# Performance work log

Measured on AMD Instinct MI355X. Metric: run time of the kernel, lower is better.

Reference implementation:

```python
import jax, jax.numpy as jnp
import numpy as np

B, S, HID, HEADS = 1, 2048, 4096, 32
HEAD_D = HID // HEADS
SCALE = float(1.0 / np.sqrt(HEAD_D))  # = 1/norm_factor^2 with use_mup=False


def setup_inputs() -> dict:
    key = jax.random.key(0)
    k0, k1, k2, k3, k4 = jax.random.split(key, 5)
    return {
        "x": jax.random.normal(k0, (B, S, HID), jnp.float32),
        "attn_qkvw": jax.random.normal(k1, (HID, 3 * HID), jnp.float32) * 0.02,
        "attn_qkvb": jax.random.normal(k2, (3 * HID,), jnp.float32) * 0.02,
        "attn_ow": jax.random.normal(k3, (HID, HID), jnp.float32) * 0.02,
        "attn_ob": jax.random.normal(k4, (HID,), jnp.float32) * 0.02,
    }


def reference(x, attn_qkvw, attn_qkvb, attn_ow, attn_ob):
    # QKV projection (LinearOp): [B,S,HID] @ [HID,3*HID] + bias -> packed qkv
    qkv = x @ attn_qkvw + attn_qkvb
    q, k, v = jnp.split(qkv, 3, axis=-1)  # each [B,S,HID]

    def to_heads(t):
        return t.reshape(B, S, HEADS, HEAD_D)

    q, k, v = to_heads(q), to_heads(k), to_heads(v)
    # flash kernel math: softmax(scale * q k^T + causal mask) @ v (numerically
    # stable online softmax == standard stable softmax)
    scores = jnp.einsum("bqhd,bkhd->bhqk", q, k) * jnp.float32(SCALE)
    causal = jnp.tril(jnp.ones((S, S), dtype=bool))  # P_SEQ = 0
    scores = jnp.where(causal[None, None], scores, jnp.float32(-jnp.inf))
    attn = jax.nn.softmax(scores, axis=-1)
    ctx = jnp.einsum("bhqk,bkhd->bqhd", attn, v).reshape(B, S, HID)
    # output projection
    return ctx @ attn_ow + attn_ob
```

## Files before the change

### kernel.cpp

```cpp
#include <hip/hip_runtime.h>
#include <hip/hip_bf16.h>
#include <math.h>

typedef __bf16 bf16_t;
typedef __bf16 bf16x8 __attribute__((ext_vector_type(8)));
typedef float f32x4 __attribute__((ext_vector_type(4)));

#define AS1 __attribute__((address_space(1)))
#define AS3 __attribute__((address_space(3)))

static constexpr int S_  = 2048;
static constexpr int HID = 4096;
static constexpr int NH  = 32;
static constexpr int HD  = 128;
static constexpr int N3  = 3 * HID;
static constexpr float SCALE = 0.08838834764831845f;

__global__ void cvt_f32_bf16(const float* __restrict__ in, bf16_t* __restrict__ out, int n4) {
  int i = blockIdx.x * blockDim.x + threadIdx.x;
  if (i >= n4) return;
  float4 v = ((const float4*)in)[i];
  union { bf16_t h[4]; short4 s4; } u;
  u.h[0] = (bf16_t)v.x; u.h[1] = (bf16_t)v.y; u.h[2] = (bf16_t)v.z; u.h[3] = (bf16_t)v.w;
  ((short4*)out)[i] = u.s4;
}

__global__ void transcvt(const float* __restrict__ in, bf16_t* __restrict__ out, int R, int C) {
  __shared__ float t[32][33];
  int r0 = blockIdx.y * 32, c0 = blockIdx.x * 32;
  int tx = threadIdx.x, ty = threadIdx.y;
#pragma unroll
  for (int i = 0; i < 32; i += 8)
    t[ty + i][tx] = in[(size_t)(r0 + ty + i) * C + c0 + tx];
  __syncthreads();
#pragma unroll
  for (int i = 0; i < 32; i += 8)
    out[(size_t)(c0 + ty + i) * R + r0 + tx] = (bf16_t)t[tx][ty + i];
}

__global__ void vtrans(const bf16_t* __restrict__ qkv, bf16_t* __restrict__ vt) {
  __shared__ bf16_t t[32][33];
  int h = blockIdx.z;
  int s0 = blockIdx.x * 32, d0 = blockIdx.y * 32;
  int tx = threadIdx.x, ty = threadIdx.y;
#pragma unroll
  for (int i = 0; i < 32; i += 8)
    t[ty + i][tx] = qkv[(size_t)(s0 + ty + i) * N3 + 2 * HID + h * HD + d0 + tx];
  __syncthreads();
#pragma unroll
  for (int i = 0; i < 32; i += 8)
    vt[(size_t)(h * HD + d0 + ty + i) * S_ + s0 + tx] = t[tx][ty + i];
}


template <bool STG, int VMC>
__device__ __forceinline__ void tile_step(
    const char* slot, int aoff, int boff,
    const bf16_t* gA, const bf16_t* gB, int kst, size_t skA,
    char* stg_dst, f32x4 (&acc)[4][4]) {
  bf16x8 a[4], b[4];
#pragma unroll
  for (int mi = 0; mi < 4; ++mi) a[mi] = *(const bf16x8*)(slot + aoff + mi * 1024);
#pragma unroll
  for (int ni = 0; ni < 4; ++ni) b[ni] = *(const bf16x8*)(slot + 16384 + boff + ni * 1024);
  if constexpr (STG) {
    __builtin_amdgcn_global_load_lds((const AS1 void*)(gA + kst), (AS3 void*)(stg_dst), 16, 0, 0);
    __builtin_amdgcn_global_load_lds((const AS1 void*)(gA + skA + kst), (AS3 void*)(stg_dst + 8192), 16, 0, 0);
    __builtin_amdgcn_global_load_lds((const AS1 void*)(gB + kst), (AS3 void*)(stg_dst + 16384), 16, 0, 0);
  }
  if constexpr (VMC == 3) asm volatile("s_waitcnt vmcnt(3)" ::: "memory");
  else if constexpr (VMC == 0) asm volatile("s_waitcnt vmcnt(0)" ::: "memory");
  __builtin_amdgcn_s_barrier();
  __builtin_amdgcn_s_setprio(1);
#pragma unroll
  for (int mi = 0; mi < 4; ++mi)
#pragma unroll
    for (int ni = 0; ni < 4; ++ni)
      acc[mi][ni] = __builtin_amdgcn_mfma_f32_16x16x32_bf16(a[mi], b[ni], acc[mi][ni], 0, 0, 0);
  __builtin_amdgcn_s_setprio(0);
  __builtin_amdgcn_s_barrier();
}

template <typename OutT>
__global__ __launch_bounds__(512, 4) void gemm_p(
    const bf16_t* __restrict__ A, const bf16_t* __restrict__ BT,
    const float* __restrict__ bias, OutT* __restrict__ C,
    int M, int N, int K) {
  extern __shared__ char smem[];
  const int tid = threadIdx.x;
  const int wv = tid >> 6, ln = tid & 63;
  const int lr = ln & 15, lg = ln >> 4;
  const int wm = wv >> 1, wn = wv & 1;

  const int nx = N >> 7;
  const int qx = gridDim.x >> 3;
  const int wg = (blockIdx.x & 7) * qx + (blockIdx.x >> 3);
  const int m0 = (wg / nx) * 256, n0 = (wg % nx) * 128;

  const int lrow = wv * 16 + (ln >> 2);
  const int lcol = ((ln & 3) << 3) ^ ((ln & 32) >> 1);
  const bf16_t* gA = A + (size_t)(m0 + lrow) * K + lcol;
  const bf16_t* gB = BT + (size_t)(n0 + lrow) * K + lcol;
  const size_t skA = (size_t)128 * K;

  const int sw = (lr & 8) << 2;
  const int aoff = (wm * 64 + lr) * 64 + ((lg * 16) ^ sw);
  const int boff = (wn * 64 + lr) * 64 + ((lg * 16) ^ sw);

  f32x4 acc[4][4] = {};

#pragma unroll
  for (int t = 0; t < 2; ++t) {
    char* d = smem + t * 24576 + wv * 1024;
    __builtin_amdgcn_global_load_lds((const AS1 void*)(gA + t * 32), (AS3 void*)(d), 16, 0, 0);
    __builtin_amdgcn_global_load_lds((const AS1 void*)(gA + skA + t * 32), (AS3 void*)(d + 8192), 16, 0, 0);
    __builtin_amdgcn_global_load_lds((const AS1 void*)(gB + t * 32), (AS3 void*)(d + 16384), 16, 0, 0);
  }
  asm volatile("s_waitcnt vmcnt(3)" ::: "memory");
  __builtin_amdgcn_s_barrier();

  const int NT = K >> 5;
  int slot = 0, nslot = 2;
  int t = 0;
  for (; t < NT - 2; ++t) {
    tile_step<true, 3>(smem + slot * 24576, aoff, boff, gA, gB, (t + 2) * 32,
                       skA, smem + nslot * 24576 + wv * 1024, acc);
    slot = (slot == 2) ? 0 : slot + 1;
    nslot = (nslot == 2) ? 0 : nslot + 1;
  }
  tile_step<false, 0>(smem + slot * 24576, aoff, boff, gA, gB, 0, skA, smem, acc);
  slot = (slot == 2) ? 0 : slot + 1;
  tile_step<false, -1>(smem + slot * 24576, aoff, boff, gA, gB, 0, skA, smem, acc);

#pragma unroll
  for (int mi = 0; mi < 4; ++mi)
#pragma unroll
    for (int ni = 0; ni < 4; ++ni) {
      const int col = n0 + wn * 64 + ni * 16 + lr;
      const float bv = bias[col];
#pragma unroll
      for (int i = 0; i < 4; ++i) {
        const int row = m0 + wm * 64 + mi * 16 + lg * 4 + i;
        C[(size_t)row * N + col] = (OutT)(acc[mi][ni][i] + bv);
      }
    }
}

__global__ __launch_bounds__(256, 4) void attn_fwd(
    const bf16_t* __restrict__ qkv, const bf16_t* __restrict__ vt,
    bf16_t* __restrict__ ctx) {
  __shared__ __align__(16) bf16_t Ks[64][136];
  __shared__ __align__(16) bf16_t Vts[128][72];

  const int tid = threadIdx.x;
  const int wv = tid >> 6, ln = tid & 63;
  bf16_t* Pl = &Ks[0][0] + wv * (16 * 72);

  const int bid = blockIdx.x;
  const int h  = ((bid & 7) << 2) + (bid >> 8);
  const int qt = 31 - ((((bid >> 3) & 31) + ((bid >> 8) << 3)) & 31);
  const int q0 = qt * 64;
  const int lr = ln & 15, lg = ln >> 4;

  bf16x8 qf[4];
#pragma unroll
  for (int kk = 0; kk < 4; ++kk) {
    bf16x8 r = *(const bf16x8*)(qkv + (size_t)(q0 + 16 * wv + lr) * N3 + h * HD + kk * 32 + lg * 8);
#pragma unroll
    for (int j = 0; j < 8; ++j) r[j] = (bf16_t)((float)r[j] * SCALE);
    qf[kk] = r;
  }

  f32x4 oacc[8] = {};
  float mrow[4], psum[4];
#pragma unroll
  for (int i = 0; i < 4; ++i) { mrow[i] = -INFINITY; psum[i] = 0.f; }

  const int ntiles = qt + 1;
  for (int t = 0; t < ntiles; ++t) {
    const int kv0 = t * 64;
    __syncthreads();
#pragma unroll
    for (int it = 0; it < 4; ++it) {
      int c = tid + it * 256;
      {
        int row = c >> 4, col = (c & 15) * 8;
        *(bf16x8*)&Ks[row][col] =
            *(const bf16x8*)(qkv + (size_t)(kv0 + row) * N3 + HID + h * HD + col);
      }
      {
        int row = c >> 3, col = (c & 7) * 8;
        *(bf16x8*)&Vts[row][col] =
            *(const bf16x8*)(vt + (size_t)(h * HD + row) * S_ + kv0 + col);
      }
    }
    __syncthreads();

    f32x4 sacc[4] = {};
#pragma unroll
    for (int kk = 0; kk < 4; ++kk)
#pragma unroll
      for (int ni = 0; ni < 4; ++ni) {
        bf16x8 kf = *(const bf16x8*)&Ks[16 * ni + lr][kk * 32 + lg * 8];
        sacc[ni] = __builtin_amdgcn_mfma_f32_16x16x32_bf16(qf[kk], kf, sacc[ni], 0, 0, 0);
      }

    const bool needmask = (kv0 + 63 > q0 + 16 * wv);
    float p[4][4];
    float mx[4];
    bool grow = false;
#pragma unroll
    for (int i = 0; i < 4; ++i) {
      const int row = q0 + 16 * wv + lg * 4 + i;
      float m_ = -INFINITY;
#pragma unroll
      for (int ni = 0; ni < 4; ++ni) {
        float s = sacc[ni][i];
        if (needmask && (kv0 + 16 * ni + lr > row)) s = -INFINITY;
        p[ni][i] = s;
        m_ = fmaxf(m_, s);
      }
      m_ = fmaxf(m_, __shfl_xor(m_, 1, 64));
      m_ = fmaxf(m_, __shfl_xor(m_, 2, 64));
      m_ = fmaxf(m_, __shfl_xor(m_, 4, 64));
      m_ = fmaxf(m_, __shfl_xor(m_, 8, 64));
      mx[i] = m_;
      grow |= (m_ > mrow[i]);
    }
    if (__any(grow)) {
      float alpha[4];
#pragma unroll
      for (int i = 0; i < 4; ++i) {
        const float mn = fmaxf(mrow[i], mx[i]);
        alpha[i] = __expf(mrow[i] - mn);
        mrow[i] = mn;
        psum[i] *= alpha[i];
      }
#pragma unroll
      for (int nf = 0; nf < 8; ++nf)
#pragma unroll
        for (int i = 0; i < 4; ++i) oacc[nf][i] *= alpha[i];
    }
#pragma unroll
    for (int i = 0; i < 4; ++i) {
      float ps = 0.f;
#pragma unroll
      for (int ni = 0; ni < 4; ++ni) {
        float e = __expf(p[ni][i] - mrow[i]);
        p[ni][i] = e;
        ps += e;
      }
      psum[i] += ps;
    }

    __syncthreads();

#pragma unroll
    for (int ni = 0; ni < 4; ++ni)
#pragma unroll
      for (int i = 0; i < 4; ++i)
        Pl[(lg * 4 + i) * 72 + 16 * ni + lr] = (bf16_t)p[ni][i];

#pragma unroll
    for (int kk2 = 0; kk2 < 2; ++kk2) {
      bf16x8 pf = *(const bf16x8*)&Pl[lr * 72 + kk2 * 32 + lg * 8];
#pragma unroll
      for (int nf = 0; nf < 8; ++nf) {
        bf16x8 vf = *(const bf16x8*)&Vts[16 * nf + lr][kk2 * 32 + lg * 8];
        oacc[nf] = __builtin_amdgcn_mfma_f32_16x16x32_bf16(pf, vf, oacc[nf], 0, 0, 0);
      }
    }
  }

#pragma unroll
  for (int i = 0; i < 4; ++i) {
    float s = psum[i];
    s += __shfl_xor(s, 1, 64);
    s += __shfl_xor(s, 2, 64);
    s += __shfl_xor(s, 4, 64);
    s += __shfl_xor(s, 8, 64);
    psum[i] = 1.f / s;
  }
#pragma unroll
  for (int nf = 0; nf < 8; ++nf)
#pragma unroll
    for (int i = 0; i < 4; ++i) {
      int row = q0 + 16 * wv + lg * 4 + i;
      int col = h * HD + 16 * nf + lr;
      ctx[(size_t)row * HID + col] = (bf16_t)(oacc[nf][i] * psum[i]);
    }
}

extern "C" void kernel_launch(void* const* d_in, const int* in_sizes, int n_in,
                              void* d_out, int out_size, void* d_ws, size_t ws_size,
                              hipStream_t stream) {
  const float* x    = (const float*)d_in[0];
  const float* wqkv = (const float*)d_in[1];
  const float* bqkv = (const float*)d_in[2];
  const float* ow   = (const float*)d_in[3];
  const float* ob   = (const float*)d_in[4];
  float* out = (float*)d_out;

  char* w = (char*)d_ws;
  bf16_t* xb    = (bf16_t*)(w);
  bf16_t* wqkvT = (bf16_t*)(w + (size_t)16777216);
  bf16_t* qkv   = (bf16_t*)(w + (size_t)117440512);
  bf16_t* vt    = (bf16_t*)(w + (size_t)167772160);
  bf16_t* ctx   = (bf16_t*)(w + (size_t)184549376);
  bf16_t* owT   = (bf16_t*)(w + (size_t)201326592);

  (void)in_sizes; (void)n_in; (void)out_size; (void)ws_size;

  cvt_f32_bf16<<<(S_ * HID / 4 + 255) / 256, 256, 0, stream>>>(x, xb, S_ * HID / 4);
  transcvt<<<dim3(N3 / 32, HID / 32), dim3(32, 8), 0, stream>>>(wqkv, wqkvT, HID, N3);
  transcvt<<<dim3(HID / 32, HID / 32), dim3(32, 8), 0, stream>>>(ow, owT, HID, HID);
  gemm_p<bf16_t><<<(S_ / 256) * (N3 / 128), 512, 73728, stream>>>(xb, wqkvT, bqkv, qkv, S_, N3, HID);
  vtrans<<<dim3(S_ / 32, HD / 32, NH), dim3(32, 8), 0, stream>>>(qkv, vt);
  attn_fwd<<<(S_ / 64) * NH, 256, 0, stream>>>(qkv, vt, ctx);
  gemm_p<float><<<(S_ / 256) * (HID / 128), 512, 73728, stream>>>(ctx, owT, ob, out, S_, HID, HID);
}
```

Before: 550.6 us.

## Double attention query tile per block and vectorize weight transpose-convert

After: 520.3 us. -5.5%, faster.

```diff
diff --git a/kernel.cpp b/kernel.cpp
--- a/kernel.cpp
+++ b/kernel.cpp
@@ -25,17 +25,30 @@
   ((short4*)out)[i] = u.s4;
 }
 
-__global__ void transcvt(const float* __restrict__ in, bf16_t* __restrict__ out, int R, int C) {
-  __shared__ float t[32][33];
-  int r0 = blockIdx.y * 32, c0 = blockIdx.x * 32;
-  int tx = threadIdx.x, ty = threadIdx.y;
-#pragma unroll
-  for (int i = 0; i < 32; i += 8)
-    t[ty + i][tx] = in[(size_t)(r0 + ty + i) * C + c0 + tx];
+__global__ __launch_bounds__(256) void transcvt64(
+    const float* __restrict__ in, bf16_t* __restrict__ out, int R, int C) {
+  __shared__ float t[64][65];
+  const int r0 = blockIdx.y * 64, c0 = blockIdx.x * 64;
+  const int tid = threadIdx.x;
+  const int rr = tid >> 4, c4 = (tid & 15) * 4;
+#pragma unroll
+  for (int it = 0; it < 4; ++it) {
+    float4 v = *(const float4*)&in[(size_t)(r0 + rr + it * 16) * C + c0 + c4];
+    t[rr + it * 16][c4 + 0] = v.x;
+    t[rr + it * 16][c4 + 1] = v.y;
+    t[rr + it * 16][c4 + 2] = v.z;
+    t[rr + it * 16][c4 + 3] = v.w;
+  }
   __syncthreads();
-#pragma unroll
-  for (int i = 0; i < 32; i += 8)
-    out[(size_t)(c0 + ty + i) * R + r0 + tx] = (bf16_t)t[tx][ty + i];
+  const int cc = tid >> 3, r8 = (tid & 7) * 8;
+#pragma unroll
+  for (int it = 0; it < 2; ++it) {
+    const int c = cc + it * 32;
+    bf16x8 w;
+#pragma unroll
+    for (int j = 0; j < 8; ++j) w[j] = (bf16_t)t[r8 + j][c];
+    *(bf16x8*)&out[(size_t)(c0 + c) * R + r0 + r8] = w;
+  }
 }
 
 __global__ void vtrans(const bf16_t* __restrict__ qkv, bf16_t* __restrict__ vt) {
@@ -51,7 +64,6 @@
   for (int i = 0; i < 32; i += 8)
     vt[(size_t)(h * HD + d0 + ty + i) * S_ + s0 + tx] = t[tx][ty + i];
 }
-
 
 template <bool STG, int VMC>
 __device__ __forceinline__ void tile_step(
@@ -146,7 +158,7 @@
     }
 }
 
-__global__ __launch_bounds__(256, 4) void attn_fwd(
+__global__ __launch_bounds__(256, 2) void attn_fwd(
     const bf16_t* __restrict__ qkv, const bf16_t* __restrict__ vt,
     bf16_t* __restrict__ ctx) {
   __shared__ __align__(16) bf16_t Ks[64][136];
@@ -154,29 +166,36 @@
 
   const int tid = threadIdx.x;
   const int wv = tid >> 6, ln = tid & 63;
-  bf16_t* Pl = &Ks[0][0] + wv * (16 * 72);
+  bf16_t* Pl = &Ks[0][0] + wv * (32 * 68);
 
   const int bid = blockIdx.x;
-  const int h  = ((bid & 7) << 2) + (bid >> 8);
-  const int qt = 31 - ((((bid >> 3) & 31) + ((bid >> 8) << 3)) & 31);
-  const int q0 = qt * 64;
+  const int a = bid >> 3;
+  const int hsub = a >> 4;
+  const int h  = ((bid & 7) << 2) + hsub;
+  const int qt = 15 - (((a & 15) + (hsub << 2)) & 15);
+  const int q0 = qt * 128;
   const int lr = ln & 15, lg = ln >> 4;
-
-  bf16x8 qf[4];
-#pragma unroll
-  for (int kk = 0; kk < 4; ++kk) {
-    bf16x8 r = *(const bf16x8*)(qkv + (size_t)(q0 + 16 * wv + lr) * N3 + h * HD + kk * 32 + lg * 8);
-#pragma unroll
-    for (int j = 0; j < 8; ++j) r[j] = (bf16_t)((float)r[j] * SCALE);
-    qf[kk] = r;
-  }
-
-  f32x4 oacc[8] = {};
-  float mrow[4], psum[4];
-#pragma unroll
-  for (int i = 0; i < 4; ++i) { mrow[i] = -INFINITY; psum[i] = 0.f; }
-
-  const int ntiles = qt + 1;
+  const int rbase = q0 + 32 * wv;
+
+  bf16x8 qf[2][4];
+#pragma unroll
+  for (int rg = 0; rg < 2; ++rg)
+#pragma unroll
+    for (int kk = 0; kk < 4; ++kk) {
+      bf16x8 r = *(const bf16x8*)(qkv + (size_t)(rbase + 16 * rg + lr) * N3 + h * HD + kk * 32 + lg * 8);
+#pragma unroll
+      for (int j = 0; j < 8; ++j) r[j] = (bf16_t)((float)r[j] * SCALE);
+      qf[rg][kk] = r;
+    }
+
+  f32x4 oacc[2][8] = {};
+  float mrow[2][4], psum[2][4];
+#pragma unroll
+  for (int rg = 0; rg < 2; ++rg)
+#pragma unroll
+    for (int i = 0; i < 4; ++i) { mrow[rg][i] = -INFINITY; psum[rg][i] = 0.f; }
+
+  const int ntiles = 2 * qt + 2;
   for (int t = 0; t < ntiles; ++t) {
     const int kv0 = t * 64;
     __syncthreads();
@@ -196,99 +215,115 @@
     }
     __syncthreads();
 
-    f32x4 sacc[4] = {};
+    f32x4 sacc[2][4] = {};
 #pragma unroll
     for (int kk = 0; kk < 4; ++kk)
 #pragma unroll
       for (int ni = 0; ni < 4; ++ni) {
         bf16x8 kf = *(const bf16x8*)&Ks[16 * ni + lr][kk * 32 + lg * 8];
-        sacc[ni] = __builtin_amdgcn_mfma_f32_16x16x32_bf16(qf[kk], kf, sacc[ni], 0, 0, 0);
-      }
-
-    const bool needmask = (kv0 + 63 > q0 + 16 * wv);
-    float p[4][4];
-    float mx[4];
+        sacc[0][ni] = __builtin_amdgcn_mfma_f32_16x16x32_bf16(qf[0][kk], kf, sacc[0][ni], 0, 0, 0);
+        sacc[1][ni] = __builtin_amdgcn_mfma_f32_16x16x32_bf16(qf[1][kk], kf, sacc[1][ni], 0, 0, 0);
+      }
+
+    float p[2][4][4];
+    float mx[2][4];
     bool grow = false;
 #pragma unroll
-    for (int i = 0; i < 4; ++i) {
-      const int row = q0 + 16 * wv + lg * 4 + i;
-      float m_ = -INFINITY;
-#pragma unroll
-      for (int ni = 0; ni < 4; ++ni) {
-        float s = sacc[ni][i];
-        if (needmask && (kv0 + 16 * ni + lr > row)) s = -INFINITY;
-        p[ni][i] = s;
-        m_ = fmaxf(m_, s);
-      }
-      m_ = fmaxf(m_, __shfl_xor(m_, 1, 64));
-      m_ = fmaxf(m_, __shfl_xor(m_, 2, 64));
-      m_ = fmaxf(m_, __shfl_xor(m_, 4, 64));
-      m_ = fmaxf(m_, __shfl_xor(m_, 8, 64));
-      mx[i] = m_;
-      grow |= (m_ > mrow[i]);
+    for (int rg = 0; rg < 2; ++rg) {
+      const bool needmask = (kv0 + 63 > rbase + 16 * rg);
+#pragma unroll
+      for (int i = 0; i < 4; ++i) {
+        const int row = rbase + 16 * rg + lg * 4 + i;
+        float m_ = -INFINITY;
+#pragma unroll
+        for (int ni = 0; ni < 4; ++ni) {
+          float s = sacc[rg][ni][i];
+          if (needmask && (kv0 + 16 * ni + lr > row)) s = -INFINITY;
+          p[rg][ni][i] = s;
+          m_ = fmaxf(m_, s);
+        }
+        m_ = fmaxf(m_, __shfl_xor(m_, 1, 64));
+        m_ = fmaxf(m_, __shfl_xor(m_, 2, 64));
+        m_ = fmaxf(m_, __shfl_xor(m_, 4, 64));
+        m_ = fmaxf(m_, __shfl_xor(m_, 8, 64));
+        mx[rg][i] = m_;
+        grow |= (m_ > mrow[rg][i]);
+      }
     }
     if (__any(grow)) {
-      float alpha[4];
+#pragma unroll
+      for (int rg = 0; rg < 2; ++rg) {
+        float alpha[4];
+#pragma unroll
+        for (int i = 0; i < 4; ++i) {
+          const float mn = fmaxf(mrow[rg][i], mx[rg][i]);
+          alpha[i] = __expf(mrow[rg][i] - mn);
+          mrow[rg][i] = mn;
+          psum[rg][i] *= alpha[i];
+        }
+#pragma unroll
+        for (int nf = 0; nf < 8; ++nf)
+#pragma unroll
+          for (int i = 0; i < 4; ++i) oacc[rg][nf][i] *= alpha[i];
+      }
+    }
+#pragma unroll
+    for (int rg = 0; rg < 2; ++rg)
 #pragma unroll
       for (int i = 0; i < 4; ++i) {
-        const float mn = fmaxf(mrow[i], mx[i]);
-        alpha[i] = __expf(mrow[i] - mn);
-        mrow[i] = mn;
-        psum[i] *= alpha[i];
-      }
-#pragma unroll
-      for (int nf = 0; nf < 8; ++nf)
-#pragma unroll
-        for (int i = 0; i < 4; ++i) oacc[nf][i] *= alpha[i];
-    }
-#pragma unroll
-    for (int i = 0; i < 4; ++i) {
-      float ps = 0.f;
-#pragma unroll
-      for (int ni = 0; ni < 4; ++ni) {
-        float e = __expf(p[ni][i] - mrow[i]);
-        p[ni][i] = e;
-        ps += e;
-      }
-      psum[i] += ps;
-    }
+        float ps = 0.f;
+#pragma unroll
+        for (int ni = 0; ni < 4; ++ni) {
+          float e = __expf(p[rg][ni][i] - mrow[rg][i]);
+          p[rg][ni][i] = e;
+          ps += e;
+        }
+        psum[rg][i] += ps;
+      }
 
     __syncthreads();
 
 #pragma unroll
-    for (int ni = 0; ni < 4; ++ni)
-#pragma unroll
-      for (int i = 0; i < 4; ++i)
-        Pl[(lg * 4 + i) * 72 + 16 * ni + lr] = (bf16_t)p[ni][i];
+    for (int rg = 0; rg < 2; ++rg)
+#pragma unroll
+      for (int ni = 0; ni < 4; ++ni)
+#pragma unroll
+        for (int i = 0; i < 4; ++i)
+          Pl[(16 * rg + lg * 4 + i) * 68 + 16 * ni + lr] = (bf16_t)p[rg][ni][i];
 
 #pragma unroll
     for (int kk2 = 0; kk2 < 2; ++kk2) {
-      bf16x8 pf = *(const bf16x8*)&Pl[lr * 72 + kk2 * 32 + lg * 8];
+      bf16x8 pf0 = *(const bf16x8*)&Pl[lr * 68 + kk2 * 32 + lg * 8];
+      bf16x8 pf1 = *(const bf16x8*)&Pl[(16 + lr) * 68 + kk2 * 32 + lg * 8];
 #pragma unroll
       for (int nf = 0; nf < 8; ++nf) {
         bf16x8 vf = *(const bf16x8*)&Vts[16 * nf + lr][kk2 * 32 + lg * 8];
-        oacc[nf] = __builtin_amdgcn_mfma_f32_16x16x32_bf16(pf, vf, oacc[nf], 0, 0, 0);
-      }
-    }
-  }
-
-#pragma unroll
-  for (int i = 0; i < 4; ++i) {
-    float s = psum[i];
-    s += __shfl_xor(s, 1, 64);
-    s += __shfl_xor(s, 2, 64);
-    s += __shfl_xor(s, 4, 64);
-    s += __shfl_xor(s, 8, 64);
-    psum[i] = 1.f / s;
-  }
-#pragma unroll
-  for (int nf = 0; nf < 8; ++nf)
+        oacc[0][nf] = __builtin_amdgcn_mfma_f32_16x16x32_bf16(pf0, vf, oacc[0][nf], 0, 0, 0);
+        oacc[1][nf] = __builtin_amdgcn_mfma_f32_16x16x32_bf16(pf1, vf, oacc[1][nf], 0, 0, 0);
+      }
+    }
+  }
+
+#pragma unroll
+  for (int rg = 0; rg < 2; ++rg) {
 #pragma unroll
     for (int i = 0; i < 4; ++i) {
-      int row = q0 + 16 * wv + lg * 4 + i;
-      int col = h * HD + 16 * nf + lr;
-      ctx[(size_t)row * HID + col] = (bf16_t)(oacc[nf][i] * psum[i]);
-    }
+      float s = psum[rg][i];
+      s += __shfl_xor(s, 1, 64);
+      s += __shfl_xor(s, 2, 64);
+      s += __shfl_xor(s, 4, 64);
+      s += __shfl_xor(s, 8, 64);
+      psum[rg][i] = 1.f / s;
+    }
+#pragma unroll
+    for (int nf = 0; nf < 8; ++nf)
+#pragma unroll
+      for (int i = 0; i < 4; ++i) {
+        int row = rbase + 16 * rg + lg * 4 + i;
+        int col = h * HD + 16 * nf + lr;
+        ctx[(size_t)row * HID + col] = (bf16_t)(oacc[rg][nf][i] * psum[rg][i]);
+      }
+  }
 }
 
 extern "C" void kernel_launch(void* const* d_in, const int* in_sizes, int n_in,
@@ -312,10 +347,10 @@
   (void)in_sizes; (void)n_in; (void)out_size; (void)ws_size;
 
   cvt_f32_bf16<<<(S_ * HID / 4 + 255) / 256, 256, 0, stream>>>(x, xb, S_ * HID / 4);
-  transcvt<<<dim3(N3 / 32, HID / 32), dim3(32, 8), 0, stream>>>(wqkv, wqkvT, HID, N3);
-  transcvt<<<dim3(HID / 32, HID / 32), dim3(32, 8), 0, stream>>>(ow, owT, HID, HID);
+  transcvt64<<<dim3(N3 / 64, HID / 64), 256, 0, stream>>>(wqkv, wqkvT, HID, N3);
+  transcvt64<<<dim3(HID / 64, HID / 64), 256, 0, stream>>>(ow, owT, HID, HID);
   gemm_p<bf16_t><<<(S_ / 256) * (N3 / 128), 512, 73728, stream>>>(xb, wqkvT, bqkv, qkv, S_, N3, HID);
   vtrans<<<dim3(S_ / 32, HD / 32, NH), dim3(32, 8), 0, stream>>>(qkv, vt);
-  attn_fwd<<<(S_ / 64) * NH, 256, 0, stream>>>(qkv, vt, ctx);
+  attn_fwd<<<(S_ / 128) * NH, 256, 0, stream>>>(qkv, vt, ctx);
   gemm_p<float><<<(S_ / 256) * (HID / 128), 512, 73728, stream>>>(ctx, owT, ob, out, S_, HID, HID);
 }
```
